# Optimization experiments

Measured on AMD Instinct MI355X. Metric: run time of the kernel, lower is better.

Reference implementation:

```python
import jax, jax.numpy as jnp
import numpy as np

D_MODEL = 1024
D_STATE = 32
D_CONV = 4
D_INNER = 2 * D_MODEL          # mamba default expand=2
DT_RANK = D_MODEL // 16        # 'auto' -> ceil(d_model/16)
BATCH, SEQ = 4, 2048
LN_EPS = 1e-5


def setup_inputs() -> dict:
    key = jax.random.key(0)
    ks = jax.random.split(key, 8)
    s = 0.02
    # S4D-real init for A_log, as in mamba_ssm
    A_log = jnp.log(jnp.tile(jnp.arange(1, D_STATE + 1, dtype=jnp.float32)[None, :], (D_INNER, 1)))
    return {
        "x": jax.random.normal(ks[0], (BATCH, SEQ, D_MODEL), jnp.float32),
        "in_proj_w": jax.random.normal(ks[1], (D_MODEL, 2 * D_INNER), jnp.float32) * s,
        "conv_w": jax.random.normal(ks[2], (D_INNER, D_CONV), jnp.float32) * s,
        "conv_b": jnp.zeros((D_INNER,), jnp.float32),
        "x_proj_w": jax.random.normal(ks[3], (D_INNER, DT_RANK + 2 * D_STATE), jnp.float32) * s,
        "dt_proj_w": jax.random.normal(ks[4], (DT_RANK, D_INNER), jnp.float32) * s,
        "dt_proj_b": jax.random.uniform(ks[5], (D_INNER,), jnp.float32, -4.0, -2.0),  # softplus -> small dt
        "A_log": A_log,
        "D": jnp.ones((D_INNER,), jnp.float32),
        "out_proj_w": jax.random.normal(ks[6], (D_INNER, D_MODEL), jnp.float32) * s,
        "ln_gamma": jnp.ones((D_MODEL,), jnp.float32),
        "ln_beta": jnp.zeros((D_MODEL,), jnp.float32),
    }


def reference(x, in_proj_w, conv_w, conv_b, x_proj_w, dt_proj_w, dt_proj_b,
              A_log, D, out_proj_w, ln_gamma, ln_beta):
    Bb, Ll, _ = x.shape
    # in_proj -> split into ssm branch (xi) and gate (z)
    xz = x @ in_proj_w                              # [B,L,2*Di]
    xi, z = jnp.split(xz, 2, axis=-1)               # each [B,L,Di]

    # causal depthwise conv1d (kernel D_CONV), left-padded, truncated to L
    xp = jnp.pad(xi, ((0, 0), (D_CONV - 1, 0), (0, 0)))
    xc = conv_b
    for k in range(D_CONV):
        xc = xc + xp[:, k:k + Ll, :] * conv_w[None, None, :, k]
    xi = jax.nn.silu(xc)                            # [B,L,Di]

    # x_proj -> dt, B, C
    dbc = xi @ x_proj_w                             # [B,L,dt_rank+2*S]
    dt = dbc[..., :DT_RANK]
    Bm = dbc[..., DT_RANK:DT_RANK + D_STATE]        # [B,L,S]
    Cm = dbc[..., DT_RANK + D_STATE:]               # [B,L,S]
    delta = jax.nn.softplus(dt @ dt_proj_w + dt_proj_b)  # [B,L,Di]

    A = -jnp.exp(A_log)                             # [Di,S]

    def step(h, inp):
        dl, bt, ct, ut = inp                        # [B,Di],[B,S],[B,S],[B,Di]
        dA = jnp.exp(dl[..., None] * A)             # [B,Di,S]
        h = dA * h + (dl * ut)[..., None] * bt[:, None, :]
        y = jnp.einsum('bds,bs->bd', h, ct)
        return h, y

    h0 = jnp.zeros((Bb, D_INNER, D_STATE), x.dtype)
    xs = (delta.transpose(1, 0, 2), Bm.transpose(1, 0, 2),
          Cm.transpose(1, 0, 2), xi.transpose(1, 0, 2))
    _, ys = jax.lax.scan(step, h0, xs)              # ys: [L,B,Di]

    y = ys.transpose(1, 0, 2) + xi * D              # skip term u*D
    y = y * jax.nn.silu(z)                          # gate
    out = y @ out_proj_w                            # [B,L,d_model]

    # LayerNorm(d_model)
    mu = out.mean(-1, keepdims=True)
    var = out.var(-1, keepdims=True)
    return (out - mu) / jnp.sqrt(var + LN_EPS) * ln_gamma + ln_beta
```

## Files before the change

kernel.cpp:

```cpp
#include <hip/hip_runtime.h>
#include <math.h>

#define D_MODEL 1024
#define D_STATE 32
#define D_CONV  4
#define D_INNER 2048
#define DT_RANK 64
#define BATCH   4
#define SEQ     2048
#define NTOK    (BATCH*SEQ)
#define DBC_N   (DT_RANK + 2*D_STATE)
#define NC      32
#define CL      (SEQ/NC)
#define KSPLIT  8
#define LOG2E   1.4426950408889634f

typedef unsigned short u16;
typedef short bf16x8 __attribute__((ext_vector_type(8)));
typedef float f32x4  __attribute__((ext_vector_type(4)));

__device__ __forceinline__ float bf2f(u16 u){
  return __uint_as_float(((unsigned)u) << 16);
}
__device__ __forceinline__ u16 f2bf(float f){
  unsigned u = __float_as_uint(f);
  return (u16)((u + 0x7fffu + ((u >> 16) & 1u)) >> 16);
}
__device__ __forceinline__ float sigmoidf_(float x){ return 1.f/(1.f+__expf(-x)); }
__device__ __forceinline__ float exp2_fast(float x){
  float r;
  asm("v_exp_f32 %0, %1" : "=v"(r) : "v"(x));
  return r;
}

typedef __attribute__((address_space(3))) void       lds_v;
typedef const __attribute__((address_space(1))) void gl_v;
#define GLOAD_LDS16(g, l) \
  __builtin_amdgcn_global_load_lds((gl_v*)(g), (lds_v*)(l), 16, 0, 0)

template<int MODE>
__global__ __launch_bounds__(256)
void mfma_gemm(int K,
               const u16* __restrict__ A, int lda,
               const u16* __restrict__ B, int ldb,
               void* __restrict__ C1, int ldc,
               u16*  __restrict__ C2,
               const float* __restrict__ bias)
{
  __shared__ u16 As[128*32];
  __shared__ u16 Bs[128*32];
  const int tid  = threadIdx.x;
  const int lane = tid & 63;
  const int wave = tid >> 6;
  const int wm = (wave>>1)*64, wn = (wave&1)*64;
  const int m0 = blockIdx.y*128, n0 = blockIdx.x*128;
  const size_t koff = (MODE==3) ? (size_t)blockIdx.z*K : 0;

  const int srow = tid >> 2;
  const int scs  = (((tid & 3) ^ ((srow >> 1) & 3)) * 8);

  const u16* Ag = A + (size_t)(m0 + srow)*lda + scs + koff;
  const u16* Bg = B + (size_t)(n0 + srow)*ldb + scs + koff;

  const int fr = lane & 15;
  const int fq = lane >> 4;
  const int sx = (fr >> 1) & 3;
  const int rdoff = ((fq ^ sx) * 8);
  f32x4 acc[4][4] = {};

  u16* as0 = &As[tid*8];
  u16* as1 = &As[2048 + tid*8];
  u16* bs0 = &Bs[tid*8];
  u16* bs1 = &Bs[2048 + tid*8];

  for (int k0=0; k0<K; k0+=32){
    GLOAD_LDS16(Ag + k0,                    as0);
    GLOAD_LDS16(Ag + (size_t)64*lda + k0,   as1);
    GLOAD_LDS16(Bg + k0,                    bs0);
    GLOAD_LDS16(Bg + (size_t)64*ldb + k0,   bs1);
    __syncthreads();

    bf16x8 af[4], bfr[4];
    #pragma unroll
    for (int i=0;i<4;i++){
      af[i]  = *(const bf16x8*)&As[(wm + i*16 + fr)*32 + rdoff];
      bfr[i] = *(const bf16x8*)&Bs[(wn + i*16 + fr)*32 + rdoff];
    }
    #pragma unroll
    for (int mi=0;mi<4;mi++)
      #pragma unroll
      for (int ni=0;ni<4;ni++)
        acc[mi][ni] = __builtin_amdgcn_mfma_f32_16x16x32_bf16(
            af[mi], bfr[ni], acc[mi][ni], 0, 0, 0);
    __syncthreads();
  }

  float* Cf = (float*)C1;
  if (MODE==3) Cf += (size_t)blockIdx.z*((size_t)NTOK*DBC_N);

  const bool second = (MODE==2) && (n0 >= D_INNER);
  #pragma unroll
  for (int mi=0;mi<4;mi++){
    #pragma unroll
    for (int ni=0;ni<4;ni++){
      int col = n0 + wn + ni*16 + fr;
      #pragma unroll
      for (int r=0;r<4;r++){
        int row = m0 + wm + mi*16 + fq*4 + r;
        float v = acc[mi][ni][r];
        if (MODE==0 || MODE==3){
          Cf[(size_t)row*ldc + col] = v;
        } else if (MODE==4){
          v += bias[col];
          v = (v > 20.f) ? v : log1pf(__expf(v));
          ((u16*)C1)[(size_t)row*ldc + col] = f2bf(v);
        } else {
          if (second) C2[(size_t)row*D_INNER + (col - D_INNER)] = f2bf(v);
          else        ((u16*)C1)[(size_t)row*D_INNER + col]     = f2bf(v);
        }
      }
    }
  }
}

__global__ __launch_bounds__(256)
void cvt_f32_bf16(const float* __restrict__ in, u16* __restrict__ out)
{
  size_t i = (size_t)blockIdx.x*256 + threadIdx.x;
  float4 v = ((const float4*)in)[i];
  ushort4 o;
  o.x=f2bf(v.x); o.y=f2bf(v.y); o.z=f2bf(v.z); o.w=f2bf(v.w);
  ((ushort4*)out)[i] = o;
}

__global__ __launch_bounds__(256)
void transpose_cvt(const float* __restrict__ in, u16* __restrict__ out,
                   int R, int C)
{
  __shared__ float tile[64][65];
  const int bc = blockIdx.x*64, br = blockIdx.y*64;
  const int tx = threadIdx.x & 63, ty = threadIdx.x >> 6;
  #pragma unroll
  for (int i=0;i<16;i++){
    int r = ty + i*4;
    tile[r][tx] = in[(size_t)(br+r)*C + bc+tx];
  }
  __syncthreads();
  #pragma unroll
  for (int i=0;i<16;i++){
    int r = ty + i*4;
    out[(size_t)(bc+r)*R + br+tx] = f2bf(tile[tx][r]);
  }
}

__global__ __launch_bounds__(256)
void reduce_pk(const float* __restrict__ part, float* __restrict__ dbc,
               u16* __restrict__ dtbf)
{
  size_t i = (size_t)blockIdx.x*256 + threadIdx.x;
  const size_t stride4 = (size_t)NTOK*DBC_N/4;
  float4 s = ((const float4*)part)[i];
  #pragma unroll
  for (int z=1; z<KSPLIT; ++z){
    float4 v = ((const float4*)part)[z*stride4 + i];
    s.x+=v.x; s.y+=v.y; s.z+=v.z; s.w+=v.w;
  }
  ((float4*)dbc)[i] = s;
  int j = (int)(i & 31);
  if (j < 16){
    size_t row = i >> 5;
    ushort4 o;
    o.x=f2bf(s.x); o.y=f2bf(s.y); o.z=f2bf(s.z); o.w=f2bf(s.w);
    *(ushort4*)(dtbf + row*DT_RANK + 4*j) = o;
  }
}

__global__ __launch_bounds__(256)
void conv_silu_kernel(const u16* __restrict__ xi_bf,
                      const float* __restrict__ conv_w,
                      const float* __restrict__ conv_b,
                      u16* __restrict__ u_bf)
{
  size_t idx = (size_t)blockIdx.x*256 + threadIdx.x;
  int d = (int)(idx % D_INNER);
  size_t bt = idx / D_INNER;
  int t = (int)(bt % SEQ);
  size_t b = bt / SEQ;
  const u16* xi = xi_bf + b*(size_t)SEQ*D_INNER;
  float accv = conv_b[d];
  #pragma unroll
  for (int k=0;k<D_CONV;k++){
    int tt = t + k - (D_CONV-1);
    if (tt >= 0) accv += bf2f(xi[(size_t)tt*D_INNER + d]) * conv_w[d*D_CONV + k];
  }
  float res = accv * sigmoidf_(accv);
  u_bf[idx] = f2bf(res);
}

__global__ __launch_bounds__(256)
void scan_part1(const float* __restrict__ dbc,
                const u16*   __restrict__ delta,
                const u16*   __restrict__ u,
                const float* __restrict__ A_log,
                float* __restrict__ q,
                float* __restrict__ sumdl_buf)
{
  const int ndg  = D_INNER/256;
  const int dgrp = blockIdx.x % ndg;
  const int c    = (blockIdx.x / ndg) % NC;
  const int b    =  blockIdx.x / (ndg*NC);
  const int d    = dgrp*256 + threadIdx.x;

  const float* Ap = A_log + (size_t)d*D_STATE;
  const float base = -__expf(Ap[0]) * LOG2E;
  bool fastp = true;
  #pragma unroll
  for (int s=1; s<D_STATE; ++s){
    float a2 = -__expf(Ap[s]) * LOG2E;
    float ideal = base * (float)(s+1);
    fastp = fastp && (fabsf(a2 - ideal) <= 1e-4f*fabsf(ideal));
  }

  const size_t tok0 = (size_t)b*SEQ + (size_t)c*CL;
  const u16*   dptr = delta + tok0*D_INNER + d;
  const u16*   uptr = u     + tok0*D_INNER + d;
  const float* dbcp = dbc   + tok0*DBC_N;

  float h[D_STATE] = {};
  float sumdl = 0.f;

  if (fastp){
    for (int t=0; t<CL; ++t){
      float dl = bf2f(dptr[(size_t)t*D_INNER]);
      float uu = bf2f(uptr[(size_t)t*D_INNER]);
      sumdl += dl;
      float w  = dl*uu;
      float E  = exp2_fast(dl*base);
      float E2 = E*E, E3 = E2*E, E4 = E2*E2;
      float P  = 1.f;
      const float4* B4 = (const float4*)(dbcp + (size_t)t*DBC_N + DT_RANK);
      #pragma unroll
      for (int g=0; g<8; ++g){
        float4 Bv = B4[g];
        float m0 = P*E, m1 = P*E2, m2 = P*E3, m3 = P*E4;
        h[4*g+0] = m0*h[4*g+0] + w*Bv.x;
        h[4*g+1] = m1*h[4*g+1] + w*Bv.y;
        h[4*g+2] = m2*h[4*g+2] + w*Bv.z;
        h[4*g+3] = m3*h[4*g+3] + w*Bv.w;
        P = m3;
      }
    }
  } else {
    float A2[D_STATE];
    #pragma unroll
    for (int g=0; g<8; ++g){
      float4 al = *(const float4*)(Ap + 4*g);
      A2[4*g+0] = -__expf(al.x)*LOG2E; A2[4*g+1] = -__expf(al.y)*LOG2E;
      A2[4*g+2] = -__expf(al.z)*LOG2E; A2[4*g+3] = -__expf(al.w)*LOG2E;
    }
    for (int t=0; t<CL; ++t){
      float dl = bf2f(dptr[(size_t)t*D_INNER]);
      float uu = bf2f(uptr[(size_t)t*D_INNER]);
      sumdl += dl;
      float w = dl*uu;
      const float4* B4 = (const float4*)(dbcp + (size_t)t*DBC_N + DT_RANK);
      #pragma unroll
      for (int g=0; g<8; ++g){
        float4 Bv = B4[g];
        h[4*g+0] = exp2_fast(dl*A2[4*g+0])*h[4*g+0] + w*Bv.x;
        h[4*g+1] = exp2_fast(dl*A2[4*g+1])*h[4*g+1] + w*Bv.y;
        h[4*g+2] = exp2_fast(dl*A2[4*g+2])*h[4*g+2] + w*Bv.z;
        h[4*g+3] = exp2_fast(dl*A2[4*g+3])*h[4*g+3] + w*Bv.w;
      }
    }
  }

  float* qp = q + (((size_t)b*NC + c)*D_INNER + d)*D_STATE;
  #pragma unroll
  for (int g=0; g<8; ++g)
    ((float4*)qp)[g] = make_float4(h[4*g+0],h[4*g+1],h[4*g+2],h[4*g+3]);
  sumdl_buf[((size_t)b*NC + c)*D_INNER + d] = sumdl;
}

__global__ __launch_bounds__(256)
void scan_combine(float* __restrict__ q,
                  const float* __restrict__ sumdl_buf,
                  const float* __restrict__ A_log)
{
  size_t idx = (size_t)blockIdx.x*256 + threadIdx.x;
  int s = (int)(idx % D_STATE);
  size_t dd = idx / D_STATE;
  int d = (int)(dd % D_INNER);
  int b = (int)(dd / D_INNER);

  const float As2 = -__expf(A_log[(size_t)d*D_STATE + s]) * LOG2E;
  float H = 0.f;
  for (int c=0; c<NC; ++c){
    size_t off = (((size_t)b*NC + c)*D_INNER + d)*D_STATE + s;
    float tmp = q[off];
    q[off] = H;
    H = exp2_fast(As2 * sumdl_buf[((size_t)b*NC + c)*D_INNER + d]) * H + tmp;
  }
}

__global__ __launch_bounds__(256)
void scan_part2(const float* __restrict__ dbc,
                const u16*   __restrict__ delta,
                const u16*   __restrict__ u,
                u16*         __restrict__ zy,
                const float* __restrict__ q,
                const float* __restrict__ A_log,
                const float* __restrict__ Dp)
{
  const int ndg  = D_INNER/256;
  const int dgrp = blockIdx.x % ndg;
  const int c    = (blockIdx.x / ndg) % NC;
  const int b    =  blockIdx.x / (ndg*NC);
  const int d    = dgrp*256 + threadIdx.x;

  const float* Ap = A_log + (size_t)d*D_STATE;
  const float base = -__expf(Ap[0]) * LOG2E;
  bool fastp = true;
  #pragma unroll
  for (int s=1; s<D_STATE; ++s){
    float a2 = -__expf(Ap[s]) * LOG2E;
    float ideal = base * (float)(s+1);
    fastp = fastp && (fabsf(a2 - ideal) <= 1e-4f*fabsf(ideal));
  }

  float h[D_STATE];
  const float* qp = q + (((size_t)b*NC + c)*D_INNER + d)*D_STATE;
  #pragma unroll
  for (int g=0; g<8; ++g){
    float4 hv = ((const float4*)qp)[g];
    h[4*g+0]=hv.x; h[4*g+1]=hv.y; h[4*g+2]=hv.z; h[4*g+3]=hv.w;
  }
  const float Dd = Dp[d];

  const size_t tok0 = (size_t)b*SEQ + (size_t)c*CL;
  const u16*   dptr = delta + tok0*D_INNER + d;
  const u16*   uptr = u     + tok0*D_INNER + d;
  u16*         zp   = zy    + tok0*D_INNER + d;
  const float* dbcp = dbc   + tok0*DBC_N;

  if (fastp){
    for (int t=0; t<CL; ++t){
      float dl = bf2f(dptr[(size_t)t*D_INNER]);
      float uu = bf2f(uptr[(size_t)t*D_INNER]);
      float zz = bf2f(zp[(size_t)t*D_INNER]);
      float w  = dl*uu;
      float E  = exp2_fast(dl*base);
      float E2 = E*E, E3 = E2*E, E4 = E2*E2;
      float P  = 1.f;
      const float4* B4 = (const float4*)(dbcp + (size_t)t*DBC_N + DT_RANK);
      const float4* C4 = B4 + 8;
      float y = 0.f;
      #pragma unroll
      for (int g=0; g<8; ++g){
        float4 Bv = B4[g];
        float4 Cv = C4[g];
        float m0 = P*E, m1 = P*E2, m2 = P*E3, m3 = P*E4;
        h[4*g+0] = m0*h[4*g+0] + w*Bv.x;  y += h[4*g+0]*Cv.x;
        h[4*g+1] = m1*h[4*g+1] + w*Bv.y;  y += h[4*g+1]*Cv.y;
        h[4*g+2] = m2*h[4*g+2] + w*Bv.z;  y += h[4*g+2]*Cv.z;
        h[4*g+3] = m3*h[4*g+3] + w*Bv.w;  y += h[4*g+3]*Cv.w;
        P = m3;
      }
      zp[(size_t)t*D_INNER] = f2bf((y + uu*Dd) * (zz * sigmoidf_(zz)));
    }
  } else {
    float A2[D_STATE];
    #pragma unroll
    for (int g=0; g<8; ++g){
      float4 al = *(const float4*)(Ap + 4*g);
      A2[4*g+0] = -__expf(al.x)*LOG2E; A2[4*g+1] = -__expf(al.y)*LOG2E;
      A2[4*g+2] = -__expf(al.z)*LOG2E; A2[4*g+3] = -__expf(al.w)*LOG2E;
    }
    for (int t=0; t<CL; ++t){
      float dl = bf2f(dptr[(size_t)t*D_INNER]);
      float uu = bf2f(uptr[(size_t)t*D_INNER]);
      float zz = bf2f(zp[(size_t)t*D_INNER]);
      float w  = dl*uu;
      const float4* B4 = (const float4*)(dbcp + (size_t)t*DBC_N + DT_RANK);
      const float4* C4 = B4 + 8;
      float y = 0.f;
      #pragma unroll
      for (int g=0; g<8; ++g){
        float4 Bv = B4[g];
        float4 Cv = C4[g];
        h[4*g+0] = exp2_fast(dl*A2[4*g+0])*h[4*g+0] + w*Bv.x;  y += h[4*g+0]*Cv.x;
        h[4*g+1] = exp2_fast(dl*A2[4*g+1])*h[4*g+1] + w*Bv.y;  y += h[4*g+1]*Cv.y;
        h[4*g+2] = exp2_fast(dl*A2[4*g+2])*h[4*g+2] + w*Bv.z;  y += h[4*g+2]*Cv.z;
        h[4*g+3] = exp2_fast(dl*A2[4*g+3])*h[4*g+3] + w*Bv.w;  y += h[4*g+3]*Cv.w;
      }
      zp[(size_t)t*D_INNER] = f2bf((y + uu*Dd) * (zz * sigmoidf_(zz)));
    }
  }
}

__global__ __launch_bounds__(256)
void ln_kernel(const float* __restrict__ in,
               float* __restrict__ out,
               const float* __restrict__ gamma,
               const float* __restrict__ beta)
{
  const int row = blockIdx.x;
  const float* p = in + (size_t)row*D_MODEL;
  float* q = out + (size_t)row*D_MODEL;
  float v[4]; float s=0.f, ss=0.f;
  #pragma unroll
  for (int i=0;i<4;i++){
    float x = p[i*256 + threadIdx.x];
    v[i]=x; s+=x; ss+=x*x;
  }
  #pragma unroll
  for (int off=32; off; off>>=1){
    s  += __shfl_xor(s,  off, 64);
    ss += __shfl_xor(ss, off, 64);
  }
  __shared__ float sw[4], ssw[4];
  const int wid = threadIdx.x >> 6;
  if ((threadIdx.x & 63) == 0){ sw[wid]=s; ssw[wid]=ss; }
  __syncthreads();
  s  = sw[0]+sw[1]+sw[2]+sw[3];
  ss = ssw[0]+ssw[1]+ssw[2]+ssw[3];
  const float mu  = s * (1.f/D_MODEL);
  const float var = ss * (1.f/D_MODEL) - mu*mu;
  const float inv = rsqrtf(var + 1e-5f);
  #pragma unroll
  for (int i=0;i<4;i++){
    int col = i*256 + threadIdx.x;
    q[col] = (v[i]-mu)*inv*gamma[col] + beta[col];
  }
}

extern "C" void kernel_launch(void* const* d_in, const int* in_sizes, int n_in,
                              void* d_out, int out_size, void* d_ws, size_t ws_size,
                              hipStream_t stream)
{
  const float* x          = (const float*)d_in[0];
  const float* in_proj_w  = (const float*)d_in[1];
  const float* conv_w     = (const float*)d_in[2];
  const float* conv_b     = (const float*)d_in[3];
  const float* x_proj_w   = (const float*)d_in[4];
  const float* dt_proj_w  = (const float*)d_in[5];
  const float* dt_proj_b  = (const float*)d_in[6];
  const float* A_log      = (const float*)d_in[7];
  const float* Dp         = (const float*)d_in[8];
  const float* out_proj_w = (const float*)d_in[9];
  const float* ln_gamma   = (const float*)d_in[10];
  const float* ln_beta    = (const float*)d_in[11];
  float* out = (float*)d_out;

  char* ws = (char*)d_ws;
  u16*   x_bf    = (u16*)  (ws + 0);
  float* pkpart  = (float*)(ws + 0);
  u16*   xi_bf   = (u16*)  (ws + (size_t) 33554432);
  float* qbuf    = (float*)(ws + (size_t) 33554432);
  u16*   u_bf    = (u16*)  (ws + (size_t) 67108864);
  u16*   zybuf   = (u16*)  (ws + (size_t)100663296);
  u16*   delta_bf= (u16*)  (ws + (size_t)134217728);
  float* dbc     = (float*)(ws + (size_t)167772160);
  u16*   dtbf    = (u16*)  (ws + (size_t)171966464);
  float* sumdl   = (float*)(ws + (size_t)173015040);
  float* preln   = (float*)(ws + (size_t)174063616);
  u16*   w_inT   = (u16*)  (ws + (size_t)207618048);
  u16*   w_outT  = (u16*)  (ws + (size_t)216006656);
  u16*   x_projT = (u16*)  (ws + (size_t)220200960);
  u16*   dt_projT= (u16*)  (ws + (size_t)220725248);

  cvt_f32_bf16<<<(NTOK*(size_t)D_MODEL)/1024, 256, 0, stream>>>(x, x_bf);
  { dim3 g(4096/64, 1024/64); transpose_cvt<<<g,256,0,stream>>>(in_proj_w,  w_inT,  1024, 4096); }
  { dim3 g(1024/64, 2048/64); transpose_cvt<<<g,256,0,stream>>>(out_proj_w, w_outT, 2048, 1024); }
  { dim3 g( 128/64, 2048/64); transpose_cvt<<<g,256,0,stream>>>(x_proj_w,   x_projT, 2048, 128); }
  { dim3 g(2048/64,   64/64); transpose_cvt<<<g,256,0,stream>>>(dt_proj_w,  dt_projT,  64, 2048); }

  {
    dim3 grid(2*D_INNER/128, NTOK/128);
    mfma_gemm<2><<<grid,256,0,stream>>>(D_MODEL,
        x_bf, D_MODEL, w_inT, D_MODEL, xi_bf, 0, zybuf, nullptr);
  }
  conv_silu_kernel<<<(NTOK*(size_t)D_INNER)/256,256,0,stream>>>(
      xi_bf, conv_w, conv_b, u_bf);

  {
    dim3 grid(DBC_N/128, NTOK/128, KSPLIT);
    mfma_gemm<3><<<grid,256,0,stream>>>(D_INNER/KSPLIT,
        u_bf, D_INNER, x_projT, D_INNER, pkpart, DBC_N, nullptr, nullptr);
    reduce_pk<<<(NTOK*(size_t)DBC_N)/1024,256,0,stream>>>(pkpart, dbc, dtbf);
  }
  {
    dim3 grid(D_INNER/128, NTOK/128);
    mfma_gemm<4><<<grid,256,0,stream>>>(DT_RANK,
        dtbf, DT_RANK, dt_projT, DT_RANK, delta_bf, D_INNER, nullptr, dt_proj_b);
  }
  {
    dim3 grid1((D_INNER/256)*NC*BATCH);
    scan_part1<<<grid1,256,0,stream>>>(dbc, delta_bf, u_bf, A_log, qbuf, sumdl);
    scan_combine<<<(BATCH*(size_t)D_INNER*D_STATE)/256,256,0,stream>>>(qbuf, sumdl, A_log);
    scan_part2<<<grid1,256,0,stream>>>(dbc, delta_bf, u_bf, zybuf, qbuf, A_log, Dp);
  }
  {
    dim3 grid(D_MODEL/128, NTOK/128);
    mfma_gemm<0><<<grid,256,0,stream>>>(D_INNER,
        zybuf, D_INNER, w_outT, D_INNER, preln, D_MODEL, nullptr, nullptr);
  }
  ln_kernel<<<NTOK,256,0,stream>>>(preln, out, ln_gamma, ln_beta);
}
```

Baseline: 588.7 us.

## Double GEMM K-tile to 64, halve x_proj split-K, vectorize conv and LayerNorm

```diff
diff --git a/kernel.cpp b/kernel.cpp
--- a/kernel.cpp
+++ b/kernel.cpp
@@ -12,12 +12,13 @@
 #define DBC_N   (DT_RANK + 2*D_STATE)
 #define NC      32
 #define CL      (SEQ/NC)
-#define KSPLIT  8
+#define KSPLIT  4
 #define LOG2E   1.4426950408889634f
 
 typedef unsigned short u16;
 typedef short bf16x8 __attribute__((ext_vector_type(8)));
 typedef float f32x4  __attribute__((ext_vector_type(4)));
+typedef u16   u16x8  __attribute__((ext_vector_type(8)));
 
 __device__ __forceinline__ float bf2f(u16 u){
   return __uint_as_float(((unsigned)u) << 16);
@@ -47,8 +48,8 @@
                u16*  __restrict__ C2,
                const float* __restrict__ bias)
 {
-  __shared__ u16 As[128*32];
-  __shared__ u16 Bs[128*32];
+  __shared__ u16 As[128*64];
+  __shared__ u16 Bs[128*64];
   const int tid  = threadIdx.x;
   const int lane = tid & 63;
   const int wave = tid >> 6;
@@ -56,42 +57,41 @@
   const int m0 = blockIdx.y*128, n0 = blockIdx.x*128;
   const size_t koff = (MODE==3) ? (size_t)blockIdx.z*K : 0;
 
-  const int srow = tid >> 2;
-  const int scs  = (((tid & 3) ^ ((srow >> 1) & 3)) * 8);
-
-  const u16* Ag = A + (size_t)(m0 + srow)*lda + scs + koff;
-  const u16* Bg = B + (size_t)(n0 + srow)*ldb + scs + koff;
+  const int srow = tid >> 3;
+  const int sch  = ((tid & 7) ^ (srow & 7)) * 8;
+
+  const u16* Ag = A + (size_t)(m0 + srow)*lda + sch + koff;
+  const u16* Bg = B + (size_t)(n0 + srow)*ldb + sch + koff;
 
   const int fr = lane & 15;
   const int fq = lane >> 4;
-  const int sx = (fr >> 1) & 3;
-  const int rdoff = ((fq ^ sx) * 8);
+  const int rkey = (fr & 7);
   f32x4 acc[4][4] = {};
 
-  u16* as0 = &As[tid*8];
-  u16* as1 = &As[2048 + tid*8];
-  u16* bs0 = &Bs[tid*8];
-  u16* bs1 = &Bs[2048 + tid*8];
-
-  for (int k0=0; k0<K; k0+=32){
-    GLOAD_LDS16(Ag + k0,                    as0);
-    GLOAD_LDS16(Ag + (size_t)64*lda + k0,   as1);
-    GLOAD_LDS16(Bg + k0,                    bs0);
-    GLOAD_LDS16(Bg + (size_t)64*ldb + k0,   bs1);
+  for (int k0=0; k0<K; k0+=64){
+    #pragma unroll
+    for (int g=0; g<4; ++g){
+      GLOAD_LDS16(Ag + (size_t)(32*g)*lda + k0, &As[g*2048 + tid*8]);
+      GLOAD_LDS16(Bg + (size_t)(32*g)*ldb + k0, &Bs[g*2048 + tid*8]);
+    }
     __syncthreads();
 
-    bf16x8 af[4], bfr[4];
     #pragma unroll
-    for (int i=0;i<4;i++){
-      af[i]  = *(const bf16x8*)&As[(wm + i*16 + fr)*32 + rdoff];
-      bfr[i] = *(const bf16x8*)&Bs[(wn + i*16 + fr)*32 + rdoff];
-    }
-    #pragma unroll
-    for (int mi=0;mi<4;mi++)
-      #pragma unroll
-      for (int ni=0;ni<4;ni++)
-        acc[mi][ni] = __builtin_amdgcn_mfma_f32_16x16x32_bf16(
-            af[mi], bfr[ni], acc[mi][ni], 0, 0, 0);
+    for (int ks=0; ks<2; ++ks){
+      const int rc = ((ks*4 + fq) ^ rkey) * 8;
+      bf16x8 af[4], bfr[4];
+      #pragma unroll
+      for (int i=0;i<4;i++){
+        af[i]  = *(const bf16x8*)&As[(wm + i*16 + fr)*64 + rc];
+        bfr[i] = *(const bf16x8*)&Bs[(wn + i*16 + fr)*64 + rc];
+      }
+      #pragma unroll
+      for (int mi=0;mi<4;mi++)
+        #pragma unroll
+        for (int ni=0;ni<4;ni++)
+          acc[mi][ni] = __builtin_amdgcn_mfma_f32_16x16x32_bf16(
+              af[mi], bfr[ni], acc[mi][ni], 0, 0, 0);
+    }
     __syncthreads();
   }
 
@@ -181,20 +181,45 @@
                       const float* __restrict__ conv_b,
                       u16* __restrict__ u_bf)
 {
-  size_t idx = (size_t)blockIdx.x*256 + threadIdx.x;
-  int d = (int)(idx % D_INNER);
-  size_t bt = idx / D_INNER;
+  size_t i8 = (size_t)blockIdx.x*256 + threadIdx.x;
+  size_t base = i8*8;
+  int d0 = (int)(base % D_INNER);
+  size_t bt = base / D_INNER;
   int t = (int)(bt % SEQ);
   size_t b = bt / SEQ;
-  const u16* xi = xi_bf + b*(size_t)SEQ*D_INNER;
-  float accv = conv_b[d];
+  const u16* xi = xi_bf + b*(size_t)SEQ*D_INNER + d0;
+
+  float accv[8];
+  #pragma unroll
+  for (int j=0;j<8;j++) accv[j] = conv_b[d0+j];
+  float4 cw[8];
+  #pragma unroll
+  for (int j=0;j<8;j++) cw[j] = *(const float4*)(conv_w + (size_t)(d0+j)*D_CONV);
+
   #pragma unroll
   for (int k=0;k<D_CONV;k++){
     int tt = t + k - (D_CONV-1);
-    if (tt >= 0) accv += bf2f(xi[(size_t)tt*D_INNER + d]) * conv_w[d*D_CONV + k];
-  }
-  float res = accv * sigmoidf_(accv);
-  u_bf[idx] = f2bf(res);
+    if (tt >= 0){
+      u16x8 v = *(const u16x8*)(xi + (size_t)tt*D_INNER);
+      const float* w = (const float*)&cw[0];
+      accv[0] += bf2f(v[0]) * ((const float*)&cw[0])[k];
+      accv[1] += bf2f(v[1]) * ((const float*)&cw[1])[k];
+      accv[2] += bf2f(v[2]) * ((const float*)&cw[2])[k];
+      accv[3] += bf2f(v[3]) * ((const float*)&cw[3])[k];
+      accv[4] += bf2f(v[4]) * ((const float*)&cw[4])[k];
+      accv[5] += bf2f(v[5]) * ((const float*)&cw[5])[k];
+      accv[6] += bf2f(v[6]) * ((const float*)&cw[6])[k];
+      accv[7] += bf2f(v[7]) * ((const float*)&cw[7])[k];
+      (void)w;
+    }
+  }
+  u16x8 o;
+  #pragma unroll
+  for (int j=0;j<8;j++){
+    float r = accv[j] * sigmoidf_(accv[j]);
+    o[j] = f2bf(r);
+  }
+  *(u16x8*)(u_bf + base) = o;
 }
 
 __global__ __launch_bounds__(256)
@@ -407,12 +432,9 @@
   const int row = blockIdx.x;
   const float* p = in + (size_t)row*D_MODEL;
   float* q = out + (size_t)row*D_MODEL;
-  float v[4]; float s=0.f, ss=0.f;
-  #pragma unroll
-  for (int i=0;i<4;i++){
-    float x = p[i*256 + threadIdx.x];
-    v[i]=x; s+=x; ss+=x*x;
-  }
+  float4 v = ((const float4*)p)[threadIdx.x];
+  float s  = v.x+v.y+v.z+v.w;
+  float ss = v.x*v.x+v.y*v.y+v.z*v.z+v.w*v.w;
   #pragma unroll
   for (int off=32; off; off>>=1){
     s  += __shfl_xor(s,  off, 64);
@@ -427,11 +449,14 @@
   const float mu  = s * (1.f/D_MODEL);
   const float var = ss * (1.f/D_MODEL) - mu*mu;
   const float inv = rsqrtf(var + 1e-5f);
-  #pragma unroll
-  for (int i=0;i<4;i++){
-    int col = i*256 + threadIdx.x;
-    q[col] = (v[i]-mu)*inv*gamma[col] + beta[col];
-  }
+  float4 gm = ((const float4*)gamma)[threadIdx.x];
+  float4 bt = ((const float4*)beta )[threadIdx.x];
+  float4 o;
+  o.x = (v.x-mu)*inv*gm.x + bt.x;
+  o.y = (v.y-mu)*inv*gm.y + bt.y;
+  o.z = (v.z-mu)*inv*gm.z + bt.z;
+  o.w = (v.w-mu)*inv*gm.w + bt.w;
+  ((float4*)q)[threadIdx.x] = o;
 }
 
 extern "C" void kernel_launch(void* const* d_in, const int* in_sizes, int n_in,
@@ -480,7 +505,7 @@
     mfma_gemm<2><<<grid,256,0,stream>>>(D_MODEL,
         x_bf, D_MODEL, w_inT, D_MODEL, xi_bf, 0, zybuf, nullptr);
   }
-  conv_silu_kernel<<<(NTOK*(size_t)D_INNER)/256,256,0,stream>>>(
+  conv_silu_kernel<<<(NTOK*(size_t)D_INNER)/2048,256,0,stream>>>(
       xi_bf, conv_w, conv_b, u_bf);
 
   {
```

After: 562.2 us. 4.5% less time.
